# Optimization experiments

Hardware: AMD Instinct MI355X
Metric: run time of the kernel (lower is better)

The kernel has to match this reference:

```python
import jax, jax.numpy as jnp
import numpy as np

B, N, S = 256, 512, 32
D_ENT, D_KEY, D_IN, D_FUNC, D_TYPE, H = 256, 32, 1024, 256, 259, 32


def _init_linear(k, out_d, in_d):
    kw, kb = jax.random.split(k)
    bound = 1.0 / np.sqrt(in_d)
    W = jax.random.uniform(kw, (out_d, in_d), minval=-bound, maxval=bound, dtype=jnp.float32)
    b = jax.random.uniform(kb, (out_d,), minval=-bound, maxval=bound, dtype=jnp.float32)
    return W, b


def setup_inputs() -> dict:
    key = jax.random.key(0)
    ks = jax.random.split(key, 16)
    inp = {
        "embedding": jax.random.normal(ks[0], (B, D_IN), jnp.float32),
        "available_unit_type_mask": (jax.random.uniform(ks[1], (B, D_TYPE)) < 0.5).astype(jnp.float32),
        "available_units_mask": jnp.ones((B, N), jnp.float32),
        "entity_embedding": jax.random.normal(ks[2], (B, N, D_ENT), jnp.float32),
        "selected_units": jax.random.randint(ks[3], (B, S), 0, N, dtype=jnp.int32),
        "end_embedding": jax.random.uniform(ks[4], (1, D_KEY), minval=-1.0, maxval=1.0, dtype=jnp.float32) / np.sqrt(D_KEY),
    }
    inp["W_key"], inp["b_key"] = _init_linear(ks[5], D_KEY, D_ENT)
    inp["W_func"], inp["b_func"] = _init_linear(ks[6], D_FUNC, D_TYPE)
    inp["W_fc1"], inp["b_fc1"] = _init_linear(ks[7], D_FUNC, D_IN)
    inp["W_fc2"], inp["b_fc2"] = _init_linear(ks[8], D_KEY, D_FUNC)
    inp["W_embed"], inp["b_embed"] = _init_linear(ks[9], D_IN, D_KEY)
    inp["W_ih"], inp["b_ih"] = _init_linear(ks[10], 4 * H, D_KEY)
    inp["W_hh"], inp["b_hh"] = _init_linear(ks[11], 4 * H, H)
    return inp


def reference(embedding, available_unit_type_mask, available_units_mask, entity_embedding,
              selected_units, end_embedding, W_key, b_key, W_func, b_func, W_fc1, b_fc1,
              W_fc2, b_fc2, W_embed, b_embed, W_ih, b_ih, W_hh, b_hh):
    Bv, Nv, _ = entity_embedding.shape
    Sv = selected_units.shape[1]
    # keys for each entity + end-flag embedding appended -> [B, N+1, key_dim]
    key_t = jnp.einsum('bnd,kd->bnk', entity_embedding, W_key) + b_key
    end = jnp.broadcast_to(end_embedding[None, :, :], (Bv, 1, end_embedding.shape[1]))
    pad_key = jnp.concatenate([key_t, end], axis=1)
    # mask: entities + end flag; teacher-forced selected positions forced to 1
    mask0 = jnp.concatenate([available_units_mask, jnp.ones((Bv, 1), available_units_mask.dtype)], axis=1)
    mask0 = mask0.at[jnp.arange(Bv)[:, None], selected_units].set(1.0)
    func_embed = jax.nn.relu(available_unit_type_mask @ W_func.T + b_func)
    inv_n = 1.0 / jnp.float32(Nv)  # split_entity_num = end_flag_index = num_units
    bidx = jnp.arange(Bv)
    # per-step selected index (dummy 0 on the final end-flag step) and validity
    sel_seq = jnp.concatenate([selected_units.T, jnp.zeros((1, Bv), selected_units.dtype)], axis=0)
    valid_seq = jnp.concatenate([jnp.ones((Sv, Bv), jnp.float32), jnp.zeros((1, Bv), jnp.float32)], axis=0)

    def step(carry, xs):
        emb, h, c, mask = carry
        sel, valid = xs
        # query = fc2(relu(fc1(emb) + func_embed))
        x = jax.nn.relu(emb @ W_fc1.T + b_fc1 + func_embed) @ W_fc2.T + b_fc2
        # one LSTM step
        gates = x @ W_ih.T + b_ih + h @ W_hh.T + b_hh
        i_g, f_g, g_g, o_g = jnp.split(gates, 4, axis=1)
        c = jax.nn.sigmoid(f_g) * c + jax.nn.sigmoid(i_g) * jnp.tanh(g_g)
        h = jax.nn.sigmoid(o_g) * jnp.tanh(c)
        # masked dot-product over keys -> logits [B, N+1]
        q = jnp.einsum('bk,bnk->bn', h, pad_key) - (1.0 - mask) * 1e9
        # mark selected unit unavailable for subsequent steps
        mask = mask.at[bidx, sel].set(jnp.where(valid > 0, 0.0, mask[bidx, sel]))
        # one-hot gather of selected key, averaged, fed back into embedding
        emb_sel = pad_key[bidx, sel] * inv_n
        emb = emb + (emb_sel @ W_embed.T + b_embed) * valid[:, None]
        return (emb, h, c, mask), q

    h0 = jnp.zeros((Bv, W_hh.shape[1]), jnp.float32)
    c0 = jnp.zeros_like(h0)
    (emb, _, _, _), logits = jax.lax.scan(step, (embedding, h0, c0, mask0), (sel_seq, valid_seq))
    logits = jnp.transpose(logits, (1, 0, 2))  # [B, S+1, N+1]
    return logits, emb
```

## Files before the change

### kernel.cpp

```cpp
#include <hip/hip_runtime.h>
#include <math.h>

#define BB_ 256
#define NN_ 512
#define SS_ 32
#define NP1 513
#define SP1 33
#define D_IN 1024
#define D_TYPE 259
#define INV_N (1.0f/512.0f)

#define N_ACT 256
#define COMB_BASE 256
#define END_BID 258
#define KEY_BASE 259
#define N_KEY 2048
#define FRONT_GRID (KEY_BASE + N_KEY)

typedef short s16x4 __attribute__((ext_vector_type(4)));
typedef short s16x8 __attribute__((ext_vector_type(8)));
typedef float f32x4 __attribute__((ext_vector_type(4)));

#if defined(__has_builtin)
#if __has_builtin(__builtin_amdgcn_rcpf)
#define FRCP(x) __builtin_amdgcn_rcpf(x)
#else
#define FRCP(x) (1.0f / (x))
#endif
#else
#define FRCP(x) (1.0f / (x))
#endif

__device__ __forceinline__ float fsig(float x) { return FRCP(1.0f + __expf(-x)); }
__device__ __forceinline__ float ftanh(float x) { return fmaf(-2.0f, FRCP(1.0f + __expf(2.0f * x)), 1.0f); }
__device__ __forceinline__ short f2bf(float f) {
    unsigned u = __float_as_uint(f);
    unsigned r = (u + 0x7FFFu + ((u >> 16) & 1u)) >> 16;
    return (short)r;
}
__device__ __forceinline__ float bf2f(short s) {
    unsigned u = ((unsigned)(unsigned short)s) << 16;
    return __uint_as_float(u);
}

__global__ __launch_bounds__(256) void front_kernel(
    const float* __restrict__ ent, const float* __restrict__ Wk,
    const float* __restrict__ bk, const float* __restrict__ endv,
    const float* __restrict__ Wemb, const float* __restrict__ bemb,
    const float* __restrict__ Wfc1, const float* __restrict__ emb0,
    const float* __restrict__ bfc1, const float* __restrict__ atm,
    const float* __restrict__ Wf, const float* __restrict__ bf,
    short* __restrict__ pkbf, float* __restrict__ WcombT,
    float* __restrict__ cbv, float* __restrict__ act_pre)
{
    __shared__ __align__(128) char u_raw[33280];
    short* a_st   = (short*)u_raw;
    float* wemb_s = (float*)(u_raw + 18688);
    float* a_lds  = (float*)u_raw;
    float* w_lds  = (float*)(u_raw + 16640);
    float* kb     = (float*)u_raw;

    const int tid = threadIdx.x;
    const int bid = blockIdx.x;
    const int lane = tid & 63, w = tid >> 6;
    const int nl = lane & 15, q = lane >> 4;

    if (bid >= KEY_BASE) {
        const size_t rowbase = (size_t)(bid - KEY_BASE) * 64;

#define KSTAGE(kc_, bi_) do {                                                     \
        _Pragma("unroll")                                                         \
        for (int p_ = 0; p_ < 4; p_++) {                                          \
            int flat_ = p_ * 256 + tid;                                           \
            int row_ = flat_ >> 4, u_ = flat_ & 15;                               \
            int gf4_ = (u_ & 8) | ((u_ ^ row_) & 7);                              \
            const float* src_ = ent + (((rowbase + (size_t)row_) << 8)            \
                                       + (kc_) * 64 + gf4_ * 4);                  \
            char* dst_ = u_raw + (bi_) * 16384 + ((p_ << 8) + (w << 6)) * 16;     \
            __builtin_amdgcn_global_load_lds(                                     \
                (const __attribute__((address_space(1))) void*)src_,              \
                (__attribute__((address_space(3))) void*)dst_, 16, 0, 0);         \
        }                                                                         \
    } while (0)

        KSTAGE(0, 0);
        KSTAGE(1, 1);

        s16x8 bfr[8][2];
#pragma unroll
        for (int s = 0; s < 8; s++)
#pragma unroll
            for (int t = 0; t < 2; t++) {
                const float* src = Wk + (size_t)(t * 16 + nl) * 256 + s * 32 + q * 8;
                float4 v0 = *(const float4*)(src);
                float4 v1 = *(const float4*)(src + 4);
                s16x8 bv;
                bv[0] = f2bf(v0.x); bv[1] = f2bf(v0.y); bv[2] = f2bf(v0.z); bv[3] = f2bf(v0.w);
                bv[4] = f2bf(v1.x); bv[5] = f2bf(v1.y); bv[6] = f2bf(v1.z); bv[7] = f2bf(v1.w);
                bfr[s][t] = bv;
            }

        f32x4 acc[2];
        acc[0] = (f32x4)0.0f; acc[1] = (f32x4)0.0f;

        const int rl = w * 16 + nl;
        const int rx = rl & 7;

        asm volatile("s_waitcnt vmcnt(4)" ::: "memory");
        __builtin_amdgcn_s_barrier();
        asm volatile("" ::: "memory");

#pragma unroll
        for (int kc = 0; kc < 4; ++kc) {
            const float* kbc = kb + (kc & 1) * 4096;
#pragma unroll
            for (int ks = 0; ks < 2; ks++) {
                int s0 = ks * 8 + ((q * 2) ^ rx);
                int s1 = ks * 8 + ((q * 2 + 1) ^ rx);
                f32x4 a0 = *(const f32x4*)&kbc[rl * 64 + s0 * 4];
                f32x4 a1 = *(const f32x4*)&kbc[rl * 64 + s1 * 4];
                s16x8 af;
                af[0] = f2bf(a0[0]); af[1] = f2bf(a0[1]); af[2] = f2bf(a0[2]); af[3] = f2bf(a0[3]);
                af[4] = f2bf(a1[0]); af[5] = f2bf(a1[1]); af[6] = f2bf(a1[2]); af[7] = f2bf(a1[3]);
                acc[0] = __builtin_amdgcn_mfma_f32_16x16x32_bf16(af, bfr[kc * 2 + ks][0], acc[0], 0, 0, 0);
                acc[1] = __builtin_amdgcn_mfma_f32_16x16x32_bf16(af, bfr[kc * 2 + ks][1], acc[1], 0, 0, 0);
            }
            if (kc < 2) {
                asm volatile("s_waitcnt lgkmcnt(0)" ::: "memory");
                __builtin_amdgcn_s_barrier();
                asm volatile("" ::: "memory");
                KSTAGE(kc + 2, kc & 1);
                asm volatile("s_waitcnt vmcnt(4)" ::: "memory");
                __builtin_amdgcn_s_barrier();
                asm volatile("" ::: "memory");
            } else if (kc == 2) {
                asm volatile("s_waitcnt vmcnt(0)" ::: "memory");
                __builtin_amdgcn_s_barrier();
                asm volatile("" ::: "memory");
            }
        }
#undef KSTAGE

        float bkv0 = bk[nl], bkv1 = bk[16 + nl];
#pragma unroll
        for (int t = 0; t < 2; t++)
#pragma unroll
            for (int r = 0; r < 4; r++) {
                int rowg = (int)rowbase + w * 16 + q * 4 + r;
                int b = rowg >> 9, n = rowg & 511;
                pkbf[((size_t)b * NP1 + n) * 32 + t * 16 + nl] =
                    f2bf(acc[t][r] + (t ? bkv1 : bkv0));
            }
    } else if (bid < N_ACT) {
        const int idx = bid;
        const int jt = idx & 15, bt = idx >> 4;
        const int bb = tid >> 4, jj = tid & 15;

#pragma unroll 4
        for (int r = 0; r < 16; r++) {
            a_lds[r * 260 + tid] = atm[(size_t)(bt * 16 + r) * D_TYPE + tid];
            w_lds[r * 260 + tid] = Wf[(size_t)(jt * 16 + r) * D_TYPE + tid];
            if (tid < 3) {
                a_lds[r * 260 + 256 + tid] = atm[(size_t)(bt * 16 + r) * D_TYPE + 256 + tid];
                w_lds[r * 260 + 256 + tid] = Wf[(size_t)(jt * 16 + r) * D_TYPE + 256 + tid];
            }
        }
        __syncthreads();
        float accf;
        {
            float f0 = 0.0f, f1 = 0.0f, f2 = 0.0f, f3 = 0.0f;
            const float4* ap = (const float4*)&a_lds[bb * 260];
            const float4* wp = (const float4*)&w_lds[jj * 260];
#pragma unroll 8
            for (int i4 = 0; i4 < 64; i4++) {
                float4 a = ap[i4]; float4 wv = wp[i4];
                f0 = fmaf(a.x, wv.x, f0); f1 = fmaf(a.y, wv.y, f1);
                f2 = fmaf(a.z, wv.z, f2); f3 = fmaf(a.w, wv.w, f3);
            }
            accf = (f0 + f1) + (f2 + f3);
            for (int i = 256; i < 259; i++) accf = fmaf(a_lds[bb * 260 + i], w_lds[jj * 260 + i], accf);
        }
        float c0 = 0.0f, c1 = 0.0f, c2 = 0.0f, c3 = 0.0f;
        for (int c = 0; c < 4; c++) {
            __syncthreads();
#pragma unroll
            for (int p = 0; p < 4; p++) {
                int l4 = p * 256 + tid;
                int r = l4 >> 6, k4 = l4 & 63;
                *(float4*)&a_lds[r * 260 + k4 * 4] =
                    *(const float4*)(emb0 + (size_t)(bt * 16 + r) * D_IN + c * 256 + k4 * 4);
                *(float4*)&w_lds[r * 260 + k4 * 4] =
                    *(const float4*)(Wfc1 + (size_t)(jt * 16 + r) * D_IN + c * 256 + k4 * 4);
            }
            __syncthreads();
#pragma unroll 8
            for (int k4 = 0; k4 < 64; k4++) {
                float4 a = *(const float4*)&a_lds[bb * 260 + k4 * 4];
                float4 wv = *(const float4*)&w_lds[jj * 260 + k4 * 4];
                c0 = fmaf(a.x, wv.x, c0); c1 = fmaf(a.y, wv.y, c1);
                c2 = fmaf(a.z, wv.z, c2); c3 = fmaf(a.w, wv.w, c3);
            }
        }
        float acc = (c0 + c1) + (c2 + c3);
        const int b = bt * 16 + bb, j = jt * 16 + jj;
        act_pre[b * 256 + j] = acc + bfc1[j] + fmaxf(accf + bf[j], 0.0f);
    } else if (bid < END_BID) {
        const int m0 = bid - COMB_BASE;
        f32x4 acc[2][3];
#pragma unroll
        for (int mt = 0; mt < 2; mt++)
#pragma unroll
            for (int t = 0; t < 3; t++) acc[mt][t] = (f32x4)0.0f;

        for (int kc = 0; kc < 16; ++kc) {
            __syncthreads();
#pragma unroll
            for (int p = 0; p < 8; p++) {
                int flat = p * 256 + tid;
                int row = flat >> 4;
                int f4 = flat & 15;
                float4 v = *(const float4*)(Wfc1 + (size_t)(m0 * 128 + row) * D_IN + kc * 64 + f4 * 4);
                s16x4 sv;
                sv[0] = f2bf(v.x); sv[1] = f2bf(v.y); sv[2] = f2bf(v.z); sv[3] = f2bf(v.w);
                *(s16x4*)&a_st[row * 72 + f4 * 4] = sv;
            }
            {
                int r = tid >> 2, c0 = tid & 3;
#pragma unroll
                for (int cc = 0; cc < 9; cc++) {
                    int col = c0 + cc * 4;
                    if (col < 33) {
                        float v = (col < 32) ? Wemb[(size_t)(kc * 64 + r) * 32 + col]
                                             : bemb[kc * 64 + r];
                        wemb_s[r * 33 + col] = v;
                    }
                }
            }
            __syncthreads();
#pragma unroll
            for (int ks = 0; ks < 2; ks++) {
                s16x8 bv[3];
#pragma unroll
                for (int t = 0; t < 3; t++) {
                    int n = t * 16 + nl;
#pragma unroll
                    for (int jj = 0; jj < 8; jj++) {
                        float v = (n < 33) ? wemb_s[(ks * 32 + q * 8 + jj) * 33 + n] : 0.0f;
                        bv[t][jj] = f2bf(v);
                    }
                }
#pragma unroll
                for (int mt = 0; mt < 2; mt++) {
                    s16x8 af = *(const s16x8*)&a_st[(w * 32 + mt * 16 + nl) * 72 + ks * 32 + q * 8];
#pragma unroll
                    for (int t = 0; t < 3; t++)
                        acc[mt][t] = __builtin_amdgcn_mfma_f32_16x16x32_bf16(af, bv[t], acc[mt][t], 0, 0, 0);
                }
            }
        }
#pragma unroll
        for (int mt = 0; mt < 2; mt++)
#pragma unroll
            for (int t = 0; t < 3; t++)
#pragma unroll
                for (int r = 0; r < 4; r++) {
                    int j = m0 * 128 + w * 32 + mt * 16 + q * 4 + r;
                    int n = t * 16 + nl;
                    if (n < 32) WcombT[j * 32 + n] = acc[mt][t][r];
                    else if (n == 32) cbv[j] = acc[mt][t][r];
                }
    } else {
        const int k = tid & 31, b0 = tid >> 5;
        short evk = f2bf(endv[k]);
        for (int b = b0; b < BB_; b += 8)
            pkbf[((size_t)b * NP1 + 512) * 32 + k] = evk;
    }
}

__global__ __launch_bounds__(256, 1) void back_kernel(
    const short* __restrict__ pkbf, const float* __restrict__ act_pre0,
    const int* __restrict__ sel, const float* __restrict__ avail,
    const float* __restrict__ Wfc2, const float* __restrict__ bfc2,
    const float* __restrict__ Wih, const float* __restrict__ bih,
    const float* __restrict__ bhh, const float* __restrict__ Whh,
    const float* __restrict__ WcombT, const float* __restrict__ cbv,
    const float* __restrict__ emb0, const float* __restrict__ Wemb,
    const float* __restrict__ bemb,
    float* __restrict__ logits, float* __restrict__ emb_out)
{
    __shared__ float S[19204];
    __shared__ int sel_l[SS_];
    float* rap_l  = S;
    float* red_l  = S + 8580;
    float* x_l    = S + 17028;
    float* cumE_l = S + 18084;
    float* ssel_l = S + 19140;
    float* xg_l   = S;
    float* h_all  = S + 4224;
    float* m0_l   = S + 8580;
    int*   tf_l   = (int*)(S + 9093);

    const int tid = threadIdx.x;
    const int b = blockIdx.x;
    const int lane = tid & 63, w = tid >> 6;
    const int nl = lane & 15, q = lane >> 4;

    if (tid < SS_) sel_l[tid] = sel[b * SS_ + tid];

    {
        const int k = tid & 31, sq = tid >> 5;
        const int sq4 = sq * 4;
        int s0 = sel[b * SS_ + sq4 + 0];
        int s1 = sel[b * SS_ + sq4 + 1];
        int s2 = sel[b * SS_ + sq4 + 2];
        int s3 = sel[b * SS_ + sq4 + 3];
        float v0 = bf2f(pkbf[((size_t)b * NP1 + s0) * 32 + k]) * INV_N;
        float v1 = bf2f(pkbf[((size_t)b * NP1 + s1) * 32 + k]) * INV_N;
        float v2 = bf2f(pkbf[((size_t)b * NP1 + s2) * 32 + k]) * INV_N;
        float v3 = bf2f(pkbf[((size_t)b * NP1 + s3) * 32 + k]) * INV_N;
        float p0 = v0, p1 = p0 + v1, p2 = p1 + v2, p3 = p2 + v3;
        x_l[sq * 32 + k] = p3;
        __syncthreads();
        float off = 0.0f;
        for (int p = 0; p < 8; p++) if (p < sq) off += x_l[p * 32 + k];
        cumE_l[(sq4 + 1) * 32 + k] = off + p0;
        cumE_l[(sq4 + 2) * 32 + k] = off + p1;
        cumE_l[(sq4 + 3) * 32 + k] = off + p2;
        cumE_l[(sq4 + 4) * 32 + k] = off + p3;
        if (tid < 32) cumE_l[tid] = 0.0f;
        if (sq == 7) ssel_l[k] = off + p3;
    }
    __syncthreads();

    {
        float wcr[32];
#pragma unroll
        for (int k4 = 0; k4 < 8; k4++) {
            float4 v = *(const float4*)(WcombT + (size_t)tid * 32 + k4 * 4);
            wcr[k4*4] = v.x; wcr[k4*4+1] = v.y; wcr[k4*4+2] = v.z; wcr[k4*4+3] = v.w;
        }
        const float cbr = cbv[tid];
        const float ap0v = act_pre0[b * 256 + tid];
        for (int t = 0; t < SP1; ++t) {
            float ap = fmaf((float)t, cbr, ap0v);
            const float4* ce = (const float4*)&cumE_l[t * 32];
#pragma unroll
            for (int k4 = 0; k4 < 8; k4++) {
                float4 e = ce[k4];
                ap = fmaf(e.x, wcr[k4*4], ap);   ap = fmaf(e.y, wcr[k4*4+1], ap);
                ap = fmaf(e.z, wcr[k4*4+2], ap); ap = fmaf(e.w, wcr[k4*4+3], ap);
            }
            rap_l[t * 260 + tid] = fmaxf(ap, 0.0f);
        }
    }
    __syncthreads();

    {
        const int seg = tid >> 5, i = tid & 31;
        float wfc2r[32];
#pragma unroll
        for (int i4 = 0; i4 < 8; i4++) {
            float4 v = *(const float4*)(Wfc2 + (size_t)i * 256 + seg * 32 + i4 * 4);
            wfc2r[i4*4] = v.x; wfc2r[i4*4+1] = v.y; wfc2r[i4*4+2] = v.z; wfc2r[i4*4+3] = v.w;
        }
        for (int t = 0; t < SP1; ++t) {
            float part = 0.0f;
            const float4* rp = (const float4*)&rap_l[t * 260 + seg * 32];
#pragma unroll
            for (int i4 = 0; i4 < 8; i4++) {
                float4 rv = rp[i4];
                part = fmaf(rv.x, wfc2r[i4*4], part);   part = fmaf(rv.y, wfc2r[i4*4+1], part);
                part = fmaf(rv.z, wfc2r[i4*4+2], part); part = fmaf(rv.w, wfc2r[i4*4+3], part);
            }
            red_l[t * 256 + seg * 32 + i] = part;
        }
    }
    __syncthreads();

    for (int p = 0; p < 5; p++) {
        int idx = p * 256 + tid;
        if (idx < SP1 * 32) {
            int t = idx >> 5, i = idx & 31;
            float x = bfc2[i];
#pragma unroll
            for (int s = 0; s < 8; s++) x += red_l[t * 256 + s * 32 + i];
            x_l[t * 32 + i] = x;
        }
    }
    __syncthreads();

    {
        const int g = tid & 127, half = tid >> 7;
        float wihr[32];
#pragma unroll
        for (int k4 = 0; k4 < 8; k4++) {
            float4 v = *(const float4*)(Wih + (size_t)g * 32 + k4 * 4);
            wihr[k4*4] = v.x; wihr[k4*4+1] = v.y; wihr[k4*4+2] = v.z; wihr[k4*4+3] = v.w;
        }
        const float bihg = bih[g] + bhh[g];
        for (int t = half; t < SP1; t += 2) {
            float gg = bihg;
            const float4* xp = (const float4*)&x_l[t * 32];
#pragma unroll
            for (int k4 = 0; k4 < 8; k4++) {
                float4 xv = xp[k4];
                gg = fmaf(xv.x, wihr[k4*4], gg);   gg = fmaf(xv.y, wihr[k4*4+1], gg);
                gg = fmaf(xv.z, wihr[k4*4+2], gg); gg = fmaf(xv.w, wihr[k4*4+3], gg);
            }
            xg_l[t * 128 + g] = gg;
        }
    }
    __syncthreads();

    if (tid < 64) {
        float whh0[32], whh1[32];
#pragma unroll
        for (int k4 = 0; k4 < 8; k4++) {
            float4 v0 = *(const float4*)(Whh + (size_t)tid * 32 + k4 * 4);
            float4 v1 = *(const float4*)(Whh + (size_t)(tid + 64) * 32 + k4 * 4);
            whh0[k4*4] = v0.x; whh0[k4*4+1] = v0.y; whh0[k4*4+2] = v0.z; whh0[k4*4+3] = v0.w;
            whh1[k4*4] = v1.x; whh1[k4*4+1] = v1.y; whh1[k4*4+2] = v1.z; whh1[k4*4+3] = v1.w;
        }
        float c = 0.0f, h = 0.0f;
        for (int t = 0; t < SP1; ++t) {
            float g0 = xg_l[t * 128 + tid];
            float g1 = xg_l[t * 128 + 64 + tid];
            if (t > 0) {
#pragma unroll
                for (int k = 0; k < 32; k++) {
                    float hk = __shfl(h, k);
                    g0 = fmaf(hk, whh0[k], g0);
                    g1 = fmaf(hk, whh1[k], g1);
                }
            }
            float og0 = __shfl_xor(g0, 32);
            float og1 = __shfl_xor(g1, 32);
            float ig = fsig(g0);
            float fg = fsig(og0);
            float gv = ftanh(g1);
            float og = fsig(og1);
            float cn = fg * c + ig * gv;
            float hn = og * ftanh(cn);
            if (tid < 32) {
                c = cn; h = hn;
                h_all[t * 32 + tid] = hn;
            }
        }
    } else {
        for (int n = tid - 64; n < NP1; n += 192) {
            float m = (n < NN_) ? avail[(size_t)b * NN_ + n] : 1.0f;
            int tf = 1000;
#pragma unroll 8
            for (int s = 0; s < SS_; s++) {
                int sv = sel_l[s];
                if (sv == n) { m = 1.0f; if (s < tf) tf = s; }
            }
            m0_l[n] = m; tf_l[n] = tf;
        }
    }
    __syncthreads();

    {
        s16x8 afr[3];
#pragma unroll
        for (int mt = 0; mt < 3; mt++) {
            int row = mt * 16 + nl;
            s16x8 av;
#pragma unroll
            for (int jj = 0; jj < 8; jj++) {
                float v = (row < SP1) ? h_all[row * 32 + q * 8 + jj] : 0.0f;
                av[jj] = f2bf(v);
            }
            afr[mt] = av;
        }
        for (int tt = w; tt < 33; tt += 4) {
            int n = tt * 16 + nl;
            bool nv = n < NP1;
            s16x8 bv = nv ? *(const s16x8*)(pkbf + ((size_t)b * NP1 + n) * 32 + q * 8) : (s16x8)0;
            f32x4 acc[3];
#pragma unroll
            for (int mt = 0; mt < 3; mt++)
                acc[mt] = __builtin_amdgcn_mfma_f32_16x16x32_bf16(afr[mt], bv, (f32x4)0.0f, 0, 0, 0);
            float m0v = nv ? m0_l[n] : 0.0f;
            int tfv = nv ? tf_l[n] : 0;
#pragma unroll
            for (int mt = 0; mt < 3; mt++)
#pragma unroll
                for (int r = 0; r < 4; r++) {
                    int t = mt * 16 + q * 4 + r;
                    if (t < SP1 && nv) {
                        float mv = (t <= tfv) ? m0v : 0.0f;
                        logits[((size_t)b * SP1 + t) * NP1 + n] = acc[mt][r] - (1.0f - mv) * 1e9f;
                    }
                }
        }
    }

#pragma unroll
    for (int p = 0; p < 4; p++) {
        int i = p * 256 + tid;
        float acc = emb0[(size_t)b * D_IN + i] + 32.0f * bemb[i];
        const float* wr = Wemb + (size_t)i * 32;
#pragma unroll
        for (int k4 = 0; k4 < 8; k4++) {
            float4 wv = *(const float4*)(wr + k4 * 4);
            acc = fmaf(ssel_l[k4*4+0], wv.x, acc);
            acc = fmaf(ssel_l[k4*4+1], wv.y, acc);
            acc = fmaf(ssel_l[k4*4+2], wv.z, acc);
            acc = fmaf(ssel_l[k4*4+3], wv.w, acc);
        }
        emb_out[(size_t)b * D_IN + i] = acc;
    }
}

extern "C" void kernel_launch(void* const* d_in, const int* in_sizes, int n_in,
                              void* d_out, int out_size, void* d_ws, size_t ws_size,
                              hipStream_t stream)
{
    (void)in_sizes; (void)n_in; (void)out_size; (void)ws_size;
    const float* embedding = (const float*)d_in[0];
    const float* atm       = (const float*)d_in[1];
    const float* avail     = (const float*)d_in[2];
    const float* ent       = (const float*)d_in[3];
    const int*   sel       = (const int*)  d_in[4];
    const float* endv      = (const float*)d_in[5];
    const float* Wk   = (const float*)d_in[6];
    const float* bk   = (const float*)d_in[7];
    const float* Wf   = (const float*)d_in[8];
    const float* bf   = (const float*)d_in[9];
    const float* Wfc1 = (const float*)d_in[10];
    const float* bfc1 = (const float*)d_in[11];
    const float* Wfc2 = (const float*)d_in[12];
    const float* bfc2 = (const float*)d_in[13];
    const float* Wemb = (const float*)d_in[14];
    const float* bemb = (const float*)d_in[15];
    const float* Wih  = (const float*)d_in[16];
    const float* bih  = (const float*)d_in[17];
    const float* Whh  = (const float*)d_in[18];
    const float* bhh  = (const float*)d_in[19];

    float* ws = (float*)d_ws;
    float* act_pre = ws;
    float* WcombT  = act_pre + BB_ * 256;
    float* cbv     = WcombT + 256 * 32;
    short* pkbf    = (short*)(cbv + 256);

    float* logits  = (float*)d_out;
    float* emb_out = logits + (size_t)BB_ * SP1 * NP1;

    front_kernel<<<FRONT_GRID, 256, 0, stream>>>(ent, Wk, bk, endv, Wemb, bemb,
                                                 Wfc1, embedding, bfc1, atm, Wf, bf,
                                                 pkbf, WcombT, cbv, act_pre);
    back_kernel<<<BB_, 256, 0, stream>>>(pkbf, act_pre, sel, avail,
                                         Wfc2, bfc2, Wih, bih, bhh, Whh,
                                         WcombT, cbv, embedding, Wemb, bemb,
                                         logits, emb_out);
}
```

Measured before the change: 298.9 us.

## Load entity rows directly into registers for key projection, dropping LDS staging

The key-projection blocks no longer stage entity tiles through LDS with global_load_lds double buffering and barriers. Each lane now loads its own 256-float row slice straight into 16 float4 registers and loads W_key fragments per k-step just before the MFMAs. This removes barriers and LDS round trips for a 128 MB streaming read. In exchange, register pressure rises and the per-lane global access pattern (32-byte chunks strided by 1 KB rows) may coalesce less well than the staged copy.

```diff
diff --git a/kernel.cpp b/kernel.cpp
--- a/kernel.cpp
+++ b/kernel.cpp
@@ -58,7 +58,6 @@
     float* wemb_s = (float*)(u_raw + 18688);
     float* a_lds  = (float*)u_raw;
     float* w_lds  = (float*)(u_raw + 16640);
-    float* kb     = (float*)u_raw;
 
     const int tid = threadIdx.x;
     const int bid = blockIdx.x;
@@ -67,90 +66,46 @@
 
     if (bid >= KEY_BASE) {
         const size_t rowbase = (size_t)(bid - KEY_BASE) * 64;
-
-#define KSTAGE(kc_, bi_) do {                                                     \
-        _Pragma("unroll")                                                         \
-        for (int p_ = 0; p_ < 4; p_++) {                                          \
-            int flat_ = p_ * 256 + tid;                                           \
-            int row_ = flat_ >> 4, u_ = flat_ & 15;                               \
-            int gf4_ = (u_ & 8) | ((u_ ^ row_) & 7);                              \
-            const float* src_ = ent + (((rowbase + (size_t)row_) << 8)            \
-                                       + (kc_) * 64 + gf4_ * 4);                  \
-            char* dst_ = u_raw + (bi_) * 16384 + ((p_ << 8) + (w << 6)) * 16;     \
-            __builtin_amdgcn_global_load_lds(                                     \
-                (const __attribute__((address_space(1))) void*)src_,              \
-                (__attribute__((address_space(3))) void*)dst_, 16, 0, 0);         \
-        }                                                                         \
-    } while (0)
-
-        KSTAGE(0, 0);
-        KSTAGE(1, 1);
-
-        s16x8 bfr[8][2];
-#pragma unroll
-        for (int s = 0; s < 8; s++)
-#pragma unroll
-            for (int t = 0; t < 2; t++) {
-                const float* src = Wk + (size_t)(t * 16 + nl) * 256 + s * 32 + q * 8;
-                float4 v0 = *(const float4*)(src);
-                float4 v1 = *(const float4*)(src + 4);
-                s16x8 bv;
-                bv[0] = f2bf(v0.x); bv[1] = f2bf(v0.y); bv[2] = f2bf(v0.z); bv[3] = f2bf(v0.w);
-                bv[4] = f2bf(v1.x); bv[5] = f2bf(v1.y); bv[6] = f2bf(v1.z); bv[7] = f2bf(v1.w);
-                bfr[s][t] = bv;
-            }
-
-        f32x4 acc[2];
-        acc[0] = (f32x4)0.0f; acc[1] = (f32x4)0.0f;
-
         const int rl = w * 16 + nl;
-        const int rx = rl & 7;
-
-        asm volatile("s_waitcnt vmcnt(4)" ::: "memory");
-        __builtin_amdgcn_s_barrier();
-        asm volatile("" ::: "memory");
-
-#pragma unroll
-        for (int kc = 0; kc < 4; ++kc) {
-            const float* kbc = kb + (kc & 1) * 4096;
-#pragma unroll
-            for (int ks = 0; ks < 2; ks++) {
-                int s0 = ks * 8 + ((q * 2) ^ rx);
-                int s1 = ks * 8 + ((q * 2 + 1) ^ rx);
-                f32x4 a0 = *(const f32x4*)&kbc[rl * 64 + s0 * 4];
-                f32x4 a1 = *(const f32x4*)&kbc[rl * 64 + s1 * 4];
-                s16x8 af;
-                af[0] = f2bf(a0[0]); af[1] = f2bf(a0[1]); af[2] = f2bf(a0[2]); af[3] = f2bf(a0[3]);
-                af[4] = f2bf(a1[0]); af[5] = f2bf(a1[1]); af[6] = f2bf(a1[2]); af[7] = f2bf(a1[3]);
-                acc[0] = __builtin_amdgcn_mfma_f32_16x16x32_bf16(af, bfr[kc * 2 + ks][0], acc[0], 0, 0, 0);
-                acc[1] = __builtin_amdgcn_mfma_f32_16x16x32_bf16(af, bfr[kc * 2 + ks][1], acc[1], 0, 0, 0);
-            }
-            if (kc < 2) {
-                asm volatile("s_waitcnt lgkmcnt(0)" ::: "memory");
-                __builtin_amdgcn_s_barrier();
-                asm volatile("" ::: "memory");
-                KSTAGE(kc + 2, kc & 1);
-                asm volatile("s_waitcnt vmcnt(4)" ::: "memory");
-                __builtin_amdgcn_s_barrier();
-                asm volatile("" ::: "memory");
-            } else if (kc == 2) {
-                asm volatile("s_waitcnt vmcnt(0)" ::: "memory");
-                __builtin_amdgcn_s_barrier();
-                asm volatile("" ::: "memory");
-            }
-        }
-#undef KSTAGE
+        const float* arow = ent + ((rowbase + (size_t)rl) << 8) + q * 8;
+
+        float4 aR[16];
+#pragma unroll
+        for (int kk = 0; kk < 8; kk++) {
+            aR[kk * 2]     = *(const float4*)(arow + kk * 32);
+            aR[kk * 2 + 1] = *(const float4*)(arow + kk * 32 + 4);
+        }
+
+        const float* brow0 = Wk + (size_t)nl * 256 + q * 8;
+        const float* brow1 = Wk + (size_t)(16 + nl) * 256 + q * 8;
+
+        f32x4 acc0 = (f32x4)0.0f, acc1 = (f32x4)0.0f;
+#pragma unroll
+        for (int kk = 0; kk < 8; kk++) {
+            float4 b00 = *(const float4*)(brow0 + kk * 32);
+            float4 b01 = *(const float4*)(brow0 + kk * 32 + 4);
+            float4 b10 = *(const float4*)(brow1 + kk * 32);
+            float4 b11 = *(const float4*)(brow1 + kk * 32 + 4);
+            s16x8 af, bf0, bf1;
+            float4 a0 = aR[kk * 2], a1 = aR[kk * 2 + 1];
+            af[0] = f2bf(a0.x); af[1] = f2bf(a0.y); af[2] = f2bf(a0.z); af[3] = f2bf(a0.w);
+            af[4] = f2bf(a1.x); af[5] = f2bf(a1.y); af[6] = f2bf(a1.z); af[7] = f2bf(a1.w);
+            bf0[0] = f2bf(b00.x); bf0[1] = f2bf(b00.y); bf0[2] = f2bf(b00.z); bf0[3] = f2bf(b00.w);
+            bf0[4] = f2bf(b01.x); bf0[5] = f2bf(b01.y); bf0[6] = f2bf(b01.z); bf0[7] = f2bf(b01.w);
+            bf1[0] = f2bf(b10.x); bf1[1] = f2bf(b10.y); bf1[2] = f2bf(b10.z); bf1[3] = f2bf(b10.w);
+            bf1[4] = f2bf(b11.x); bf1[5] = f2bf(b11.y); bf1[6] = f2bf(b11.z); bf1[7] = f2bf(b11.w);
+            acc0 = __builtin_amdgcn_mfma_f32_16x16x32_bf16(af, bf0, acc0, 0, 0, 0);
+            acc1 = __builtin_amdgcn_mfma_f32_16x16x32_bf16(af, bf1, acc1, 0, 0, 0);
+        }
 
         float bkv0 = bk[nl], bkv1 = bk[16 + nl];
 #pragma unroll
-        for (int t = 0; t < 2; t++)
-#pragma unroll
-            for (int r = 0; r < 4; r++) {
-                int rowg = (int)rowbase + w * 16 + q * 4 + r;
-                int b = rowg >> 9, n = rowg & 511;
-                pkbf[((size_t)b * NP1 + n) * 32 + t * 16 + nl] =
-                    f2bf(acc[t][r] + (t ? bkv1 : bkv0));
-            }
+        for (int r = 0; r < 4; r++) {
+            int rowg = (int)rowbase + w * 16 + q * 4 + r;
+            int b = rowg >> 9, n = rowg & 511;
+            pkbf[((size_t)b * NP1 + n) * 32 + nl]      = f2bf(acc0[r] + bkv0);
+            pkbf[((size_t)b * NP1 + n) * 32 + 16 + nl] = f2bf(acc1[r] + bkv1);
+        }
     } else if (bid < N_ACT) {
         const int idx = bid;
         const int jt = idx & 15, bt = idx >> 4;
```

New measurement: 334.6 us. +11.9%, slower.
